# Optimization experiments

Measured on AMD Instinct MI355X. Metric: run time of the kernel, lower is better.

Reference implementation:

```python
import jax, jax.numpy as jnp
import numpy as np

DIM = 1024
INNER = int(DIM * 1.5)
EPS = 1e-6


def setup_inputs() -> dict:
    key = jax.random.key(0)
    ks = jax.random.split(key, 8)
    B, L, D = 4, 2048, DIM
    s1 = 1.0 / np.sqrt(D)
    s2 = 1.0 / np.sqrt(INNER)
    return {
        "x": jax.random.normal(ks[0], (B, L, D), jnp.float32),
        "W1": jax.random.normal(ks[1], (D, INNER), jnp.float32) * s1,
        "b1": jnp.zeros((INNER,), jnp.float32),
        "W2": jax.random.normal(ks[2], (INNER, 3 * D), jnp.float32) * s2,
        "b2": jnp.zeros((3 * D,), jnp.float32),
        "Wv": jax.random.normal(ks[3], (D, D), jnp.float32) * (0.5 * s1),
        "bv": jnp.zeros((D,), jnp.float32),
        "mix_weight": jnp.full((D,), 0.5, jnp.float32),
        "norm_weight": jnp.ones((D,), jnp.float32),
    }


def rmsnorm(x, w):
    norm = jnp.sqrt(jnp.mean(x * x, axis=-1, keepdims=True) + EPS)
    return x / norm * w


def reference(x, W1, b1, W2, b2, Wv, bv, mix_weight, norm_weight):
    B, L, D = x.shape
    h = jax.nn.silu(x @ W1 + b1)              # [B,L,inner]
    qkg = h @ W2 + b2                          # [B,L,3D]
    q, k, g = jnp.split(qkg, 3, axis=-1)
    scores = jnp.einsum('bld,bmd->blm', q, k) / jnp.sqrt(jnp.float32(D))
    attn = jax.nn.softmax(scores, axis=-1)
    v = (x @ Wv + bv) * jax.nn.sigmoid(g)      # gated values [B,L,D]
    global_info = jnp.einsum('blm,bmd->bld', attn, v)
    output = mix_weight * global_info + (1.0 - mix_weight) * x
    return rmsnorm(output, norm_weight)
```

## Files before the change

### kernel.cpp

```cpp
#include <hip/hip_runtime.h>
#include <hip/hip_bf16.h>
#include <stdint.h>


typedef __bf16 bf16x8 __attribute__((ext_vector_type(8)));
typedef float f32x4 __attribute__((ext_vector_type(4)));

#define VM4 asm volatile("s_waitcnt vmcnt(4)" ::: "memory")
#define VM2 asm volatile("s_waitcnt vmcnt(2)" ::: "memory")
#define VM0 asm volatile("s_waitcnt vmcnt(0)" ::: "memory")
#define LGKM0 asm volatile("s_waitcnt lgkmcnt(0)" ::: "memory")
#define BAR __builtin_amdgcn_s_barrier()
#define SCB __builtin_amdgcn_sched_barrier(0)

__device__ __forceinline__ unsigned short f2bf(float f) {
    unsigned int u = __float_as_uint(f);
    u += 0x7fffu + ((u >> 16) & 1u);
    return (unsigned short)(u >> 16);
}
__device__ __forceinline__ float bf2f(unsigned short s) {
    return __uint_as_float(((unsigned int)s) << 16);
}
__device__ __forceinline__ void llds16(const void* g, void* l) {
    __builtin_amdgcn_global_load_lds(
        (const __attribute__((address_space(1))) void*)g,
        (__attribute__((address_space(3))) void*)l, 16, 0, 0);
}
__device__ __forceinline__ f32x4 MF(bf16x8 a, bf16x8 b, f32x4 c) {
    return __builtin_amdgcn_mfma_f32_16x16x32_bf16(a, b, c, 0, 0, 0);
}

__global__ __launch_bounds__(256) void zero_f32(float* __restrict__ p, int n) {
    int i = blockIdx.x * 256 + threadIdx.x;
    if (i < n) p[i] = 0.f;
}

__global__ __launch_bounds__(256) void cvt_f32_bf16(
    const float* __restrict__ in, unsigned short* __restrict__ out, long long n8) {
    long long i = (long long)blockIdx.x * 256 + threadIdx.x;
    if (i >= n8) return;
    float4 a = ((const float4*)in)[2 * i];
    float4 b = ((const float4*)in)[2 * i + 1];
    ushort4 p0, p1;
    p0.x = f2bf(a.x); p0.y = f2bf(a.y); p0.z = f2bf(a.z); p0.w = f2bf(a.w);
    p1.x = f2bf(b.x); p1.y = f2bf(b.y); p1.z = f2bf(b.z); p1.w = f2bf(b.w);
    ((ushort4*)out)[2 * i] = p0;
    ((ushort4*)out)[2 * i + 1] = p1;
}

__global__ __launch_bounds__(256) void transpose_cvt(
    const float* __restrict__ in, unsigned short* __restrict__ out, int R, int C) {
    __shared__ unsigned short tile[32][33];
    int c0 = blockIdx.x * 32, r0 = blockIdx.y * 32;
    int cc = threadIdx.x & 31, rr = threadIdx.x >> 5;
#pragma unroll
    for (int p = 0; p < 4; ++p) {
        int r = rr + p * 8;
        tile[r][cc] = f2bf(in[(size_t)(r0 + r) * C + c0 + cc]);
    }
    __syncthreads();
#pragma unroll
    for (int p = 0; p < 4; ++p) {
        int c = rr + p * 8;
        out[(size_t)(c0 + c) * R + r0 + cc] = tile[cc][c];
    }
}

template <int EPI>
__global__ __launch_bounds__(512, 1) void gemm5(
    const unsigned short* __restrict__ A, int lda, long long Abs,
    const unsigned short* __restrict__ B, int ldb, long long Bbs,
    int K,
    void* __restrict__ out, int ldo, long long Obs,
    const float* __restrict__ bias,
    const unsigned short* __restrict__ gate, int ldg,
    float scale, int gx,
    const float* __restrict__ bnd, float* __restrict__ stat) {
    __shared__ unsigned short lds[49152];
    const int tid = threadIdx.x, lane = tid & 63, wid = tid >> 6;
    const int wr = wid >> 1, wc = wid & 1;
    const int nwg = gridDim.x;
    const int bswz = ((int)blockIdx.x & 7) * (nwg >> 3) + ((int)blockIdx.x >> 3);
    const int bx = bswz % gx, by = bswz / gx;
    const int bm = by * 256, bn = bx * 128;
    const int z = blockIdx.z;
    A += (long long)z * Abs;
    B += (long long)z * Bbs;
    const int NT = K >> 6;

    const int sswz = ((tid & 7) ^ ((tid >> 3) & 7)) * 8;
    size_t agc[4], bgc[2];
#pragma unroll
    for (int c = 0; c < 4; ++c)
        agc[c] = (size_t)(bm + c * 64 + (tid >> 3)) * lda + sswz;
#pragma unroll
    for (int c = 0; c < 2; ++c)
        bgc[c] = (size_t)(bn + c * 64 + (tid >> 3)) * ldb + sswz;
    const int wl = wid * 512;

    auto stA01 = [&](int t, int buf) {
        const size_t k0 = (size_t)t << 6;
        llds16(A + agc[0] + k0, &lds[buf + wl]);
        llds16(A + agc[1] + k0, &lds[buf + 4096 + wl]);
    };
    auto stA23 = [&](int t, int buf) {
        const size_t k0 = (size_t)t << 6;
        llds16(A + agc[2] + k0, &lds[buf + 8192 + wl]);
        llds16(A + agc[3] + k0, &lds[buf + 12288 + wl]);
    };
    auto stB = [&](int t, int buf) {
        const size_t k0 = (size_t)t << 6;
        llds16(B + bgc[0] + k0, &lds[buf + 16384 + wl]);
        llds16(B + bgc[1] + k0, &lds[buf + 20480 + wl]);
    };

    const int l15 = lane & 15, g4 = lane >> 4, l7 = lane & 7;
    const int x0 = (g4 ^ l7) * 8, x1 = ((4 + g4) ^ l7) * 8;
    const int ab = (wr * 64 + l15) * 64;
    const int bbv = 16384 + (wc * 64 + l15) * 64;
    constexpr int X = 0, Y = 24576;

    f32x4 acc[4][4] = {};

    stB(0, X); stA01(0, X); stA23(0, X); stB(1, Y);
    VM4;
    BAR; SCB;

    int t = 0;
    while (true) {
        const bool last = (t + 2) >= NT;
        bf16x8 bf[4][2], af[2][2];
#pragma unroll
        for (int j = 0; j < 4; ++j) {
            bf[j][0] = *(const bf16x8*)&lds[X + bbv + j * 1024 + x0];
            bf[j][1] = *(const bf16x8*)&lds[X + bbv + j * 1024 + x1];
        }
#pragma unroll
        for (int i = 0; i < 2; ++i) {
            af[i][0] = *(const bf16x8*)&lds[X + ab + i * 1024 + x0];
            af[i][1] = *(const bf16x8*)&lds[X + ab + i * 1024 + x1];
        }
        stA01(t + 1, Y);
        LGKM0; SCB;
        __builtin_amdgcn_s_setprio(1);
#pragma unroll
        for (int s = 0; s < 2; ++s)
#pragma unroll
            for (int i = 0; i < 2; ++i)
#pragma unroll
                for (int j = 0; j < 4; ++j)
                    acc[i][j] = MF(af[i][s], bf[j][s], acc[i][j]);
        __builtin_amdgcn_s_setprio(0);
        VM4;
        BAR; SCB;
#pragma unroll
        for (int i = 0; i < 2; ++i) {
            af[i][0] = *(const bf16x8*)&lds[X + ab + (2 + i) * 1024 + x0];
            af[i][1] = *(const bf16x8*)&lds[X + ab + (2 + i) * 1024 + x1];
        }
        stA23(t + 1, Y);
        if (!last) stB(t + 2, X);
        LGKM0; SCB;
        __builtin_amdgcn_s_setprio(1);
#pragma unroll
        for (int s = 0; s < 2; ++s)
#pragma unroll
            for (int i = 0; i < 2; ++i)
#pragma unroll
                for (int j = 0; j < 4; ++j)
                    acc[2 + i][j] = MF(af[i][s], bf[j][s], acc[2 + i][j]);
        __builtin_amdgcn_s_setprio(0);
        if (last) { VM2; } else { VM4; }
        BAR; SCB;
#pragma unroll
        for (int j = 0; j < 4; ++j) {
            bf[j][0] = *(const bf16x8*)&lds[Y + bbv + j * 1024 + x0];
            bf[j][1] = *(const bf16x8*)&lds[Y + bbv + j * 1024 + x1];
        }
#pragma unroll
        for (int i = 0; i < 2; ++i) {
            af[i][0] = *(const bf16x8*)&lds[Y + ab + i * 1024 + x0];
            af[i][1] = *(const bf16x8*)&lds[Y + ab + i * 1024 + x1];
        }
        if (!last) stA01(t + 2, X);
        LGKM0; SCB;
        __builtin_amdgcn_s_setprio(1);
#pragma unroll
        for (int s = 0; s < 2; ++s)
#pragma unroll
            for (int i = 0; i < 2; ++i)
#pragma unroll
                for (int j = 0; j < 4; ++j)
                    acc[i][j] = MF(af[i][s], bf[j][s], acc[i][j]);
        __builtin_amdgcn_s_setprio(0);
        if (last) { VM0; } else { VM4; }
        BAR; SCB;
#pragma unroll
        for (int i = 0; i < 2; ++i) {
            af[i][0] = *(const bf16x8*)&lds[Y + ab + (2 + i) * 1024 + x0];
            af[i][1] = *(const bf16x8*)&lds[Y + ab + (2 + i) * 1024 + x1];
        }
        if (!last) { stA23(t + 2, X); stB(t + 3, Y); }
        LGKM0; SCB;
        __builtin_amdgcn_s_setprio(1);
#pragma unroll
        for (int s = 0; s < 2; ++s)
#pragma unroll
            for (int i = 0; i < 2; ++i)
#pragma unroll
                for (int j = 0; j < 4; ++j)
                    acc[2 + i][j] = MF(af[i][s], bf[j][s], acc[2 + i][j]);
        __builtin_amdgcn_s_setprio(0);
        if (last) break;
        VM4;
        BAR; SCB;
        t += 2;
    }

    const int row0 = bm + wr * 64, col0 = bn + wc * 64;
    if constexpr (EPI == 1) {
        unsigned short* o = (unsigned short*)out;
#pragma unroll
        for (int i = 0; i < 4; ++i) {
            const int mb = row0 + i * 16 + g4 * 4;
#pragma unroll
            for (int j = 0; j < 4; ++j) {
                const int n = col0 + j * 16 + l15;
                const float bs = bias[n];
#pragma unroll
                for (int q = 0; q < 4; ++q)
                    o[(size_t)(mb + q) * ldo + n] = f2bf(acc[i][j][q] + bs);
            }
        }
    } else if constexpr (EPI == 2) {
        unsigned short* o = (unsigned short*)out;
#pragma unroll
        for (int i = 0; i < 4; ++i) {
            const int mb = row0 + i * 16 + g4 * 4;
#pragma unroll
            for (int j = 0; j < 4; ++j) {
                const int n = col0 + j * 16 + l15;
                const float bs = bias[n];
                ushort4 pk;
                unsigned short* pku = (unsigned short*)&pk;
#pragma unroll
                for (int q = 0; q < 4; ++q) {
                    int m = mb + q;
                    float g = bf2f(gate[(size_t)m * ldg + n]);
                    pku[q] = f2bf((acc[i][j][q] + bs) / (1.f + __expf(-g)));
                }
                size_t oi = ((size_t)(mb >> 11) * 1024 + n) * 2048 + (mb & 2047);
                *(ushort4*)(o + oi) = pk;
            }
        }
    } else if constexpr (EPI == 5) {
        unsigned short* o = (unsigned short*)out + (size_t)z * Obs;
#pragma unroll
        for (int i = 0; i < 4; ++i) {
            const int mb = row0 + i * 16 + g4 * 4;
            float rs[4] = {0.f, 0.f, 0.f, 0.f};
#pragma unroll
            for (int j = 0; j < 4; ++j) {
                const int n = col0 + j * 16 + l15;
#pragma unroll
                for (int q = 0; q < 4; ++q) {
                    float p = __expf(fminf(acc[i][j][q] * scale, 80.f));
                    o[(size_t)(mb + q) * ldo + n] = f2bf(p);
                    rs[q] += p;
                }
            }
#pragma unroll
            for (int q = 0; q < 4; ++q) {
                float s = rs[q];
                s += __shfl_xor(s, 1); s += __shfl_xor(s, 2);
                s += __shfl_xor(s, 4); s += __shfl_xor(s, 8);
                if (l15 == 0) atomicAdd(&stat[(size_t)z * 2048 + mb + q], s);
            }
        }
    } else {
        unsigned short* o = (unsigned short*)out + (size_t)z * Obs;
        const float* ls = bnd + (size_t)z * 2048;
#pragma unroll
        for (int i = 0; i < 4; ++i) {
            const int mb = row0 + i * 16 + g4 * 4;
            float invl[4];
#pragma unroll
            for (int q = 0; q < 4; ++q) invl[q] = 1.f / ls[mb + q];
#pragma unroll
            for (int j = 0; j < 4; ++j) {
                const int n = col0 + j * 16 + l15;
#pragma unroll
                for (int q = 0; q < 4; ++q)
                    o[(size_t)(mb + q) * ldo + n] = f2bf(acc[i][j][q] * invl[q]);
            }
        }
    }
}

template <int EPI>
__global__ __launch_bounds__(256, 3) void gemmk(
    const unsigned short* __restrict__ A, int lda,
    const unsigned short* __restrict__ B, int ldb,
    int K, void* __restrict__ out, int ldo,
    const float* __restrict__ bias, int gx) {
    __shared__ unsigned short lds[24576];
    const int tid = threadIdx.x, lane = tid & 63, wid = tid >> 6;
    const int nwg = gridDim.x;
    const int bswz = ((int)blockIdx.x & 7) * (nwg >> 3) + ((int)blockIdx.x >> 3);
    const int bx = bswz % gx, by = bswz / gx;
    const int bm = by * 128, bn = bx * 128;
    const int NT = K >> 5;

    const int srow = tid >> 2;
    const int sswz = ((tid & 3) ^ ((tid >> 3) & 3)) * 8;
    size_t ag[2], bg[2];
    ag[0] = (size_t)(bm + srow) * lda + sswz;
    ag[1] = (size_t)(bm + 64 + srow) * lda + sswz;
    bg[0] = (size_t)(bn + srow) * ldb + sswz;
    bg[1] = (size_t)(bn + 64 + srow) * ldb + sswz;
    const int wl = wid * 512;

    auto stage = [&](int t, int bb) {
        const size_t k0 = (size_t)t << 5;
        llds16(A + ag[0] + k0, &lds[bb + wl]);
        llds16(A + ag[1] + k0, &lds[bb + 2048 + wl]);
        llds16(B + bg[0] + k0, &lds[bb + 4096 + wl]);
        llds16(B + bg[1] + k0, &lds[bb + 6144 + wl]);
    };

    const int wr = wid >> 1, wc = wid & 1;
    const int l15 = lane & 15, g4 = lane >> 4;
    const int fswz = (g4 ^ ((l15 >> 1) & 3)) * 8;
    const int aoff = (wr * 64 + l15) * 32 + fswz;
    const int boff = 4096 + (wc * 64 + l15) * 32 + fswz;

    f32x4 acc[4][4] = {};
    stage(0, 0);
    stage(1, 8192);
    VM4; BAR;

    int bb = 0;
    for (int t = 0; t < NT; ++t) {
        const bool st = (t + 2) < NT;
        if (st) {
            const int tgt = (bb >= 8192) ? bb - 8192 : bb + 16384;
            stage(t + 2, tgt);
        }
        SCB;
        bf16x8 af[4], bf[4];
#pragma unroll
        for (int i = 0; i < 4; ++i) {
            af[i] = *(const bf16x8*)&lds[bb + aoff + i * 512];
            bf[i] = *(const bf16x8*)&lds[bb + boff + i * 512];
        }
#pragma unroll
        for (int i = 0; i < 4; ++i)
#pragma unroll
            for (int j = 0; j < 4; ++j)
                acc[i][j] = MF(af[i], bf[j], acc[i][j]);
        LGKM0;
        if (st) { VM4; } else { VM0; }
        BAR;
        bb = (bb == 16384) ? 0 : bb + 8192;
    }

    const int row0 = bm + wr * 64, col0 = bn + wc * 64;
#pragma unroll
    for (int i = 0; i < 4; ++i) {
#pragma unroll
        for (int j = 0; j < 4; ++j) {
            const int n = col0 + j * 16 + l15;
            const int mb = row0 + i * 16 + g4 * 4;
            f32x4 v = acc[i][j];
            float bs = bias[n];
            unsigned short* o = (unsigned short*)out;
#pragma unroll
            for (int q = 0; q < 4; ++q) {
                float val = v[q] + bs;
                if constexpr (EPI == 0) val = val / (1.f + __expf(-val));
                o[(size_t)(mb + q) * ldo + n] = f2bf(val);
            }
        }
    }
}

__global__ __launch_bounds__(256) void mix_rmsnorm(
    const unsigned short* __restrict__ gi, const float* __restrict__ x,
    const float* __restrict__ mixw, const float* __restrict__ normw,
    float* __restrict__ out) {
    const int D = 1024;
    const size_t base = (size_t)blockIdx.x * D;
    const int t = threadIdx.x, lane = t & 63, wid = t >> 6;
    ushort4 g4 = ((const ushort4*)(gi + base))[t];
    float4 xv = ((const float4*)(x + base))[t];
    float4 mw = ((const float4*)mixw)[t];
    float4 v;
    v.x = mw.x * bf2f(g4.x) + (1.f - mw.x) * xv.x;
    v.y = mw.y * bf2f(g4.y) + (1.f - mw.y) * xv.y;
    v.z = mw.z * bf2f(g4.z) + (1.f - mw.z) * xv.z;
    v.w = mw.w * bf2f(g4.w) + (1.f - mw.w) * xv.w;
    float ss = v.x * v.x + v.y * v.y + v.z * v.z + v.w * v.w;
#pragma unroll
    for (int off = 32; off; off >>= 1) ss += __shfl_xor(ss, off);
    __shared__ float red[4];
    if (lane == 0) red[wid] = ss;
    __syncthreads();
    ss = red[0] + red[1] + red[2] + red[3];
    float sc = rsqrtf(ss / (float)D + 1e-6f);
    float4 wv = ((const float4*)normw)[t];
    v.x *= sc * wv.x; v.y *= sc * wv.y; v.z *= sc * wv.z; v.w *= sc * wv.w;
    ((float4*)(out + base))[t] = v;
}

extern "C" void kernel_launch(void* const* d_in, const int* in_sizes, int n_in,
                              void* d_out, int out_size, void* d_ws, size_t ws_size,
                              hipStream_t stream) {
    const float* x = (const float*)d_in[0];
    const float* W1 = (const float*)d_in[1];
    const float* b1 = (const float*)d_in[2];
    const float* W2 = (const float*)d_in[3];
    const float* b2 = (const float*)d_in[4];
    const float* Wv = (const float*)d_in[5];
    const float* bv = (const float*)d_in[6];
    const float* mixw = (const float*)d_in[7];
    const float* normw = (const float*)d_in[8];
    float* out = (float*)d_out;

    const int L = 2048, D = 1024, INNER = 1536, BN4 = 4;
    const int M = BN4 * L;

    char* w = (char*)d_ws;
    auto carve = [&](size_t bytes) {
        void* p = (void*)w;
        w += (bytes + 255) & ~(size_t)255;
        return p;
    };
    unsigned short* xbf = (unsigned short*)carve((size_t)M * D * 2);
    unsigned short* w1t = (unsigned short*)carve((size_t)INNER * D * 2);
    unsigned short* w2t = (unsigned short*)carve((size_t)3 * D * INNER * 2);
    unsigned short* wvt = (unsigned short*)carve((size_t)D * D * 2);
    unsigned short* h = (unsigned short*)carve((size_t)M * INNER * 2);
    unsigned short* qkg = (unsigned short*)carve((size_t)M * 3 * D * 2);
    unsigned short* vt = (unsigned short*)carve((size_t)BN4 * D * L * 2);
    unsigned short* pbuf = (unsigned short*)carve((size_t)BN4 * L * L * 2);
    float* lsum = (float*)carve((size_t)M * 4);
    unsigned short* gi = h;

    zero_f32<<<M / 256, 256, 0, stream>>>(lsum, M);
    cvt_f32_bf16<<<(M * D) / 2048, 256, 0, stream>>>(x, xbf, (long long)M * D / 8);
    transpose_cvt<<<dim3(INNER / 32, D / 32), 256, 0, stream>>>(W1, w1t, D, INNER);
    transpose_cvt<<<dim3(3 * D / 32, INNER / 32), 256, 0, stream>>>(W2, w2t, INNER, 3 * D);
    transpose_cvt<<<dim3(D / 32, D / 32), 256, 0, stream>>>(Wv, wvt, D, D);
    gemmk<0><<<dim3(768, 1, 1), 256, 0, stream>>>(xbf, D, w1t, D, D, h, INNER,
                                                  b1, 12);
    gemm5<1><<<dim3(768, 1, 1), 512, 0, stream>>>(
        h, INNER, 0, w2t, INNER, 0, INNER, qkg, 3 * D, 0, b2, nullptr, 0,
        1.f, 24, nullptr, nullptr);
    gemm5<2><<<dim3(256, 1, 1), 512, 0, stream>>>(
        xbf, D, 0, wvt, D, 0, D, vt, L, 0, bv, qkg + 2 * D, 3 * D,
        1.f, 8, nullptr, nullptr);
    gemm5<5><<<dim3(128, 1, BN4), 512, 0, stream>>>(
        qkg, 3 * D, (long long)L * 3 * D, qkg + D, 3 * D, (long long)L * 3 * D,
        D, pbuf, L, (long long)L * L, nullptr, nullptr, 0,
        0.03125f, 16, nullptr, lsum);
    gemm5<6><<<dim3(64, 1, BN4), 512, 0, stream>>>(
        pbuf, L, (long long)L * L, vt, L, (long long)D * L, L, gi, D,
        (long long)L * D, nullptr, nullptr, 0, 1.f, 8, lsum, nullptr);
    mix_rmsnorm<<<M, 256, 0, stream>>>(gi, x, mixw, normw, out);
}
```

Measured before the change: 274.2 us.

## Use 256x256-tile GEMM kernel for QK^T scores with fused exp epilogue

Adds a dedicated gemm8 kernel for the attention-score GEMM. It uses a 256x256 output tile with 8 waves in a 2x4 layout, a double-buffered LDS pipeline of 128KB, and loads staged across quarter-steps. This replaces the 128-tile gemm5<5> launch, halving the grid from 128 to 64 blocks per batch. The aim is more operand reuse per LDS load and fewer redundant global reads, at the cost of more registers, more LDS, and fewer workgroups to fill the CUs.

```diff
diff --git a/kernel.cpp b/kernel.cpp
--- a/kernel.cpp
+++ b/kernel.cpp
@@ -63,6 +63,143 @@
     for (int p = 0; p < 4; ++p) {
         int c = rr + p * 8;
         out[(size_t)(c0 + c) * R + r0 + cc] = tile[cc][c];
+    }
+}
+
+__global__ __launch_bounds__(512, 1) void gemm8(
+    const unsigned short* __restrict__ A, int lda, long long Abs,
+    const unsigned short* __restrict__ B, int ldb, long long Bbs,
+    int K,
+    unsigned short* __restrict__ out, int ldo, long long Obs,
+    float scale, int gx, float* __restrict__ stat) {
+    __shared__ unsigned short lds[65536];
+    const int tid = threadIdx.x, lane = tid & 63, wid = tid >> 6;
+    const int wr = wid >> 2, wc = wid & 3;
+    const int nwg = gridDim.x;
+    const int bswz = ((int)blockIdx.x & 7) * (nwg >> 3) + ((int)blockIdx.x >> 3);
+    const int bx = bswz % gx, by = bswz / gx;
+    const int bm = by * 256, bn = bx * 256;
+    const int z = blockIdx.z;
+    A += (long long)z * Abs;
+    B += (long long)z * Bbs;
+    const int NT = K >> 6;
+
+    const int sswz = ((tid & 7) ^ ((tid >> 3) & 7)) * 8;
+    size_t agc[4], bgc[4];
+#pragma unroll
+    for (int c = 0; c < 4; ++c) {
+        agc[c] = (size_t)(bm + c * 64 + (tid >> 3)) * lda + sswz;
+        bgc[c] = (size_t)(bn + c * 64 + (tid >> 3)) * ldb + sswz;
+    }
+    const int wl = wid * 512;
+
+    auto stA = [&](int t, int h, int buf) {
+        const size_t k0 = (size_t)t << 6;
+        llds16(A + agc[h * 2] + k0, &lds[buf + (h * 2) * 4096 + wl]);
+        llds16(A + agc[h * 2 + 1] + k0, &lds[buf + (h * 2 + 1) * 4096 + wl]);
+    };
+    auto stB = [&](int t, int h, int buf) {
+        const size_t k0 = (size_t)t << 6;
+        llds16(B + bgc[h * 2] + k0, &lds[buf + 16384 + (h * 2) * 4096 + wl]);
+        llds16(B + bgc[h * 2 + 1] + k0,
+               &lds[buf + 16384 + (h * 2 + 1) * 4096 + wl]);
+    };
+
+    const int l15 = lane & 15, g4 = lane >> 4, l7 = lane & 7;
+    const int x0 = (g4 ^ l7) * 8, x1 = ((4 + g4) ^ l7) * 8;
+    const int ab = (wr * 128 + l15) * 64;
+    const int bbv = 16384 + (wc * 64 + l15) * 64;
+    constexpr int X = 0, Y = 32768;
+
+    f32x4 acc[8][4] = {};
+
+    stA(0, 0, X); stA(0, 1, X); stB(0, 0, X); stB(0, 1, X);
+    stB(1, 0, Y); stB(1, 1, Y);
+    VM4;
+    BAR; SCB;
+
+    int t = 0;
+    while (true) {
+        const bool st2 = (t + 2) < NT;
+#pragma unroll
+        for (int hb = 0; hb < 2; ++hb) {
+            const int buf = hb ? Y : X;
+            bf16x8 bfr[4][2];
+#pragma unroll
+            for (int q = 0; q < 4; ++q) {
+                if (q == 0) {
+#pragma unroll
+                    for (int j = 0; j < 4; ++j) {
+                        bfr[j][0] = *(const bf16x8*)&lds[buf + bbv + j * 1024 + x0];
+                        bfr[j][1] = *(const bf16x8*)&lds[buf + bbv + j * 1024 + x1];
+                    }
+                }
+                bf16x8 af[2][2];
+#pragma unroll
+                for (int mq = 0; mq < 2; ++mq) {
+                    af[mq][0] =
+                        *(const bf16x8*)&lds[buf + ab + (q * 2 + mq) * 1024 + x0];
+                    af[mq][1] =
+                        *(const bf16x8*)&lds[buf + ab + (q * 2 + mq) * 1024 + x1];
+                }
+                if (hb == 0) {
+                    if (q == 0) stA(t + 1, 0, Y);
+                    else if (q == 1) stA(t + 1, 1, Y);
+                    else if (q == 2) { if (st2) stB(t + 2, 0, X); }
+                    else { if (st2) stB(t + 2, 1, X); }
+                } else {
+                    if (q == 0) { if (st2) stA(t + 2, 0, X); }
+                    else if (q == 1) { if (st2) stA(t + 2, 1, X); }
+                    else if (q == 2) { if (st2) stB(t + 3, 0, Y); }
+                    else { if (st2) stB(t + 3, 1, Y); }
+                }
+                BAR;
+                LGKM0; SCB;
+                __builtin_amdgcn_s_setprio(1);
+#pragma unroll
+                for (int s = 0; s < 2; ++s)
+#pragma unroll
+                    for (int mq = 0; mq < 2; ++mq)
+#pragma unroll
+                        for (int j = 0; j < 4; ++j)
+                            acc[q * 2 + mq][j] =
+                                MF(af[mq][s], bfr[j][s], acc[q * 2 + mq][j]);
+                __builtin_amdgcn_s_setprio(0);
+                if (q == 3) {
+                    if (hb == 0) { if (st2) { VM4; } else { VM0; } }
+                    else if (st2) { VM4; }
+                }
+                if (hb == 1 && q == 3 && !st2) break;
+                BAR; SCB;
+            }
+        }
+        if (!st2) break;
+        t += 2;
+    }
+
+    const int row0 = bm + wr * 128, col0 = bn + wc * 64;
+    unsigned short* o = out + (size_t)z * Obs;
+#pragma unroll
+    for (int m = 0; m < 8; ++m) {
+        const int mb = row0 + m * 16 + g4 * 4;
+        float rs[4] = {0.f, 0.f, 0.f, 0.f};
+#pragma unroll
+        for (int j = 0; j < 4; ++j) {
+            const int n = col0 + j * 16 + l15;
+#pragma unroll
+            for (int qq = 0; qq < 4; ++qq) {
+                float p = __expf(fminf(acc[m][j][qq] * scale, 80.f));
+                o[(size_t)(mb + qq) * ldo + n] = f2bf(p);
+                rs[qq] += p;
+            }
+        }
+#pragma unroll
+        for (int qq = 0; qq < 4; ++qq) {
+            float s = rs[qq];
+            s += __shfl_xor(s, 1); s += __shfl_xor(s, 2);
+            s += __shfl_xor(s, 4); s += __shfl_xor(s, 8);
+            if (l15 == 0) atomicAdd(&stat[(size_t)z * 2048 + mb + qq], s);
+        }
     }
 }
 
@@ -253,30 +390,6 @@
                 *(ushort4*)(o + oi) = pk;
             }
         }
-    } else if constexpr (EPI == 5) {
-        unsigned short* o = (unsigned short*)out + (size_t)z * Obs;
-#pragma unroll
-        for (int i = 0; i < 4; ++i) {
-            const int mb = row0 + i * 16 + g4 * 4;
-            float rs[4] = {0.f, 0.f, 0.f, 0.f};
-#pragma unroll
-            for (int j = 0; j < 4; ++j) {
-                const int n = col0 + j * 16 + l15;
-#pragma unroll
-                for (int q = 0; q < 4; ++q) {
-                    float p = __expf(fminf(acc[i][j][q] * scale, 80.f));
-                    o[(size_t)(mb + q) * ldo + n] = f2bf(p);
-                    rs[q] += p;
-                }
-            }
-#pragma unroll
-            for (int q = 0; q < 4; ++q) {
-                float s = rs[q];
-                s += __shfl_xor(s, 1); s += __shfl_xor(s, 2);
-                s += __shfl_xor(s, 4); s += __shfl_xor(s, 8);
-                if (l15 == 0) atomicAdd(&stat[(size_t)z * 2048 + mb + q], s);
-            }
-        }
     } else {
         unsigned short* o = (unsigned short*)out + (size_t)z * Obs;
         const float* ls = bnd + (size_t)z * 2048;
@@ -459,10 +572,9 @@
     gemm5<2><<<dim3(256, 1, 1), 512, 0, stream>>>(
         xbf, D, 0, wvt, D, 0, D, vt, L, 0, bv, qkg + 2 * D, 3 * D,
         1.f, 8, nullptr, nullptr);
-    gemm5<5><<<dim3(128, 1, BN4), 512, 0, stream>>>(
+    gemm8<<<dim3(64, 1, BN4), 512, 0, stream>>>(
         qkg, 3 * D, (long long)L * 3 * D, qkg + D, 3 * D, (long long)L * 3 * D,
-        D, pbuf, L, (long long)L * L, nullptr, nullptr, 0,
-        0.03125f, 16, nullptr, lsum);
+        D, pbuf, L, (long long)L * L, 0.03125f, 8, lsum);
     gemm5<6><<<dim3(64, 1, BN4), 512, 0, stream>>>(
         pbuf, L, (long long)L * L, vt, L, (long long)D * L, L, gi, D,
         (long long)L * D, nullptr, nullptr, 0, 1.f, 8, lsum, nullptr);
```

Result: no change. 270.7 us (-1.3%).
